# Performance work log

Measured on AMD Instinct MI355X. Metric: run time of the kernel, lower is better.

Reference implementation:

```python
import jax, jax.numpy as jnp
import numpy as np

BETA = 1.0  # temperature; label_softmax=True


def _criterion(pred, labels):
    # pred, labels: [M, W]; KLDivLoss(log_softmax(pred*beta), softmax(labels*beta)), mean over dim 1
    log_pt = jax.nn.log_softmax(pred * BETA, axis=1)
    log_lab = jax.nn.log_softmax(labels * BETA, axis=1)
    lab = jnp.exp(log_lab)
    kl = lab * (log_lab - log_pt)
    return kl.mean(axis=1)  # [M]


def _topk_rate(epoch):
    # cosine rampdown from epoch-210 over 30 epochs, clipped to [0.8, 1]
    cur = float(np.clip(epoch - 210, 0.0, 30.0))
    r = 0.5 * (np.cos(np.pi * cur / 30.0) + 1.0)
    return float(np.clip(r, 0.8, 1.0))


def setup_inputs() -> dict:
    key = jax.random.key(0)
    ks = jax.random.split(key, 6)
    N, K, W = 1024, 17, 512  # batch, joints, SimCC bins (256*2)
    return {
        "pred_x": jax.random.normal(ks[0], (N, K, W), jnp.float32),
        "pred_y": jax.random.normal(ks[1], (N, K, W), jnp.float32),
        "gt_x": jax.random.normal(ks[2], (N, K, W), jnp.float32),
        "gt_y": jax.random.normal(ks[3], (N, K, W), jnp.float32),
        "target_weight": jax.random.uniform(ks[4], (N, K), jnp.float32),
        "use_labels": jax.random.randint(ks[5], (N,), 0, 2),
        "epoch": 225,
    }


def reference(pred_x, pred_y, gt_x, gt_y, target_weight, use_labels, epoch):
    N, K, _ = pred_x.shape
    # target_weight_real: keep rows where use_labels == 0, else zero
    weight_real = (target_weight * (use_labels == 0).astype(target_weight.dtype)[:, None]).reshape(-1)
    rate = _topk_rate(int(epoch))
    num_visible = int(jnp.count_nonzero(target_weight))
    k = int(num_visible * rate)  # static k for top-k (data-dependent, computed eagerly)

    loss_all = jnp.zeros((), pred_x.dtype)
    weight_outs = []
    for pred, gt in ((pred_x, gt_x), (pred_y, gt_y)):
        p2 = pred.reshape(-1, pred.shape[-1])   # [N*K, W]
        t2 = gt.reshape(-1, gt.shape[-1])       # [N*K, W]
        # detached pass used only to pick the k smallest per-joint losses
        loss_small = _criterion(jax.lax.stop_gradient(p2), jax.lax.stop_gradient(t2))  # [N*K]
        loss_bat = loss_small.reshape(N, K)
        loss_new = jnp.where(target_weight > 0, loss_bat, loss_small.max())
        _, topk_idx = jax.lax.top_k(-loss_new.reshape(-1), k)  # smallest-k indices
        mask = jnp.zeros(N * K, dtype=pred.dtype).at[topk_idx].set(1.0)
        # live pass (gradients flow through pred and gt)
        loss_sm_re = _criterion(p2, t2)  # [N*K]
        weight_all = 2.0 * weight_real + mask
        weight_outs.append(weight_all)
        loss_all = loss_all + (loss_sm_re * weight_all).sum()
    return (loss_all / K, weight_outs[0], weight_outs[1])
```

## Files before the change

kernel.cpp:

```cpp
#include <hip/hip_runtime.h>
#include <math.h>

#define EQCAP 2048
#define PI_D 3.141592653589793

__device__ inline float wred_max(float v) {
    #pragma unroll
    for (int o = 32; o; o >>= 1) v = fmaxf(v, __shfl_xor(v, o));
    return v;
}
__device__ inline float wred_sum(float v) {
    #pragma unroll
    for (int o = 32; o; o >>= 1) v += __shfl_xor(v, o);
    return v;
}
__device__ inline unsigned fflip(float f) {
    unsigned b = __float_as_uint(f);
    return (b & 0x80000000u) ? ~b : (b | 0x80000000u);
}

__global__ void k_init(double* acc, int* count, unsigned* gmax_u, int* eqc) {
    if (threadIdx.x == 0) {
        *acc = 0.0; *count = 0;
        gmax_u[0] = 0u; gmax_u[1] = 0u;
        eqc[0] = 0; eqc[1] = 0;
    }
}

__global__ __launch_bounds__(256) void k_loss(
    const float* __restrict__ px, const float* __restrict__ py,
    const float* __restrict__ gx, const float* __restrict__ gy,
    float* __restrict__ lossbuf, int M)
{
    int wid  = (blockIdx.x * blockDim.x + threadIdx.x) >> 6;
    int lane = threadIdx.x & 63;
    if (wid >= 2 * M) return;
    int ax  = wid >= M;
    int row = ax ? wid - M : wid;
    const float* p = ax ? py : px;
    const float* g = ax ? gy : gx;
    const float4* p4 = reinterpret_cast<const float4*>(p + (size_t)row * 512);
    const float4* g4 = reinterpret_cast<const float4*>(g + (size_t)row * 512);
    float4 pa = p4[lane], pb = p4[lane + 64];
    float4 ga = g4[lane], gb = g4[lane + 64];
    float pv[8] = {pa.x, pa.y, pa.z, pa.w, pb.x, pb.y, pb.z, pb.w};
    float gv[8] = {ga.x, ga.y, ga.z, ga.w, gb.x, gb.y, gb.z, gb.w};

    float mp = -INFINITY, mg = -INFINITY;
    #pragma unroll
    for (int i = 0; i < 8; i++) { mp = fmaxf(mp, pv[i]); mg = fmaxf(mg, gv[i]); }
    mp = wred_max(mp); mg = wred_max(mg);

    float sp = 0.f, sg = 0.f;
    #pragma unroll
    for (int i = 0; i < 8; i++) { sp += __expf(pv[i] - mp); sg += __expf(gv[i] - mg); }
    sp = wred_sum(sp); sg = wred_sum(sg);
    float lp = __logf(sp), lg = __logf(sg);

    float acc = 0.f;
    #pragma unroll
    for (int i = 0; i < 8; i++) {
        float lsg = (gv[i] - mg) - lg;
        float lsp = (pv[i] - mp) - lp;
        acc += __expf(lsg) * (lsg - lsp);
    }
    acc = wred_sum(acc);
    if (lane == 0) lossbuf[wid] = acc * (1.0f / 512.0f);
}

__global__ __launch_bounds__(256) void k_stats2(
    const float* __restrict__ tw, const float* __restrict__ lossbuf,
    int* __restrict__ count, unsigned* __restrict__ gmax_u, int M)
{
    int tid = threadIdx.x, lane = tid & 63, wv = tid >> 6;
    int j = blockIdx.x * 256 + tid;
    int c = 0; unsigned ux = 0u, uy = 0u;
    if (j < M) {
        c  = (tw[j] != 0.0f);
        ux = fflip(lossbuf[j]);
        uy = fflip(lossbuf[M + j]);
    }
    #pragma unroll
    for (int o = 32; o; o >>= 1) {
        c += __shfl_xor(c, o);
        ux = max(ux, (unsigned)__shfl_xor((int)ux, o));
        uy = max(uy, (unsigned)__shfl_xor((int)uy, o));
    }
    __shared__ int sc[4]; __shared__ unsigned sx[4], sy[4];
    if (lane == 0) { sc[wv] = c; sx[wv] = ux; sy[wv] = uy; }
    __syncthreads();
    if (tid == 0) {
        int cs = sc[0] + sc[1] + sc[2] + sc[3];
        unsigned xs = max(max(sx[0], sx[1]), max(sx[2], sx[3]));
        unsigned ys = max(max(sy[0], sy[1]), max(sy[2], sy[3]));
        if (cs) atomicAdd(count, cs);
        atomicMax(&gmax_u[0], xs);
        atomicMax(&gmax_u[1], ys);
    }
}

__global__ __launch_bounds__(1024) void k_select(
    const float* __restrict__ tw, const float* __restrict__ lossbuf,
    const int* __restrict__ count, const unsigned* __restrict__ gmax_u,
    const int* __restrict__ ep,
    int* __restrict__ ki, unsigned* __restrict__ thr_u, int* __restrict__ cless, int M)
{
    extern __shared__ unsigned keys[];
    int ax = blockIdx.x;
    int tid = threadIdx.x, lane = tid & 63, wv = tid >> 6;
    __shared__ int hist[256];
    __shared__ unsigned s_pref;
    __shared__ int s_kr, s_cl;
    __shared__ int wsum[4];

    if (tid == 0) {
        int c = *count;
        double cur = fmin(fmax((double)(ep[0] - 210), 0.0), 30.0);
        double r = 0.5 * (cos(PI_D * cur / 30.0) + 1.0);
        r = fmin(fmax(r, 0.8), 1.0);
        int k = (int)((double)c * r);
        s_kr = k; s_pref = 0u; s_cl = 0;
        if (ax == 0) *ki = k;
    }

    unsigned gmu = gmax_u[ax];
    const float* lb = lossbuf + (size_t)ax * M;
    for (int j = tid; j < M; j += 1024) {
        float t = tw[j];
        float l = lb[j];
        keys[j] = (t > 0.f) ? fflip(l) : gmu;
    }
    __syncthreads();

    int k0 = s_kr;
    if (k0 <= 0) { if (tid == 0) { thr_u[ax] = 0u; cless[ax] = 0; } return; }

    const unsigned mhi[4] = {0x00000000u, 0xFF000000u, 0xFFFF0000u, 0xFFFFFF00u};

    for (int pass = 0; pass < 4; ++pass) {
        int shift = 24 - 8 * pass;
        if (tid < 256) hist[tid] = 0;
        __syncthreads();
        unsigned m = mhi[pass];
        unsigned pref = s_pref;
        for (int j = tid; j < M; j += 1024) {
            unsigned v = keys[j];
            if ((v & m) == (pref & m)) atomicAdd(&hist[(v >> shift) & 255], 1);
        }
        __syncthreads();
        int kr = s_kr;
        int h = (tid < 256) ? hist[tid] : 0;
        int inc = h;
        #pragma unroll
        for (int o = 1; o < 64; o <<= 1) {
            int n = __shfl_up(inc, o);
            if (lane >= o) inc += n;
        }
        if (lane == 63 && wv < 4) wsum[wv] = inc;
        __syncthreads();
        if (tid < 256) {
            int off = 0;
            #pragma unroll
            for (int w = 0; w < 4; w++) if (w < wv) off += wsum[w];
            int incl = inc + off, excl = incl - h;
            if (excl < kr && incl >= kr) {
                s_pref |= ((unsigned)tid) << shift;
                s_kr = kr - excl;
                s_cl += excl;
            }
        }
        __syncthreads();
    }
    if (tid == 0) { thr_u[ax] = s_pref; cless[ax] = s_cl; }
}

__global__ __launch_bounds__(256) void k_weight(
    const float* __restrict__ tw, const int* __restrict__ ul,
    const float* __restrict__ lossbuf, const unsigned* __restrict__ gmax_u,
    float* __restrict__ outw, const int* __restrict__ ki,
    const unsigned* __restrict__ thr_u, int* __restrict__ eqc,
    int* __restrict__ eqlist, double* __restrict__ acc, int M, int Kj)
{
    int ax = blockIdx.y;
    int m = blockIdx.x * blockDim.x + threadIdx.x;
    double contrib = 0.0;
    if (m < M) {
        int k = *ki;
        float mask = 0.f;
        unsigned v = (tw[m] > 0.f) ? fflip(lossbuf[(size_t)ax * M + m]) : gmax_u[ax];
        unsigned t = thr_u[ax];
        if (k > 0) {
            if (v < t) mask = 1.f;
            else if (v == t) {
                int pos = atomicAdd(&eqc[ax], 1);
                if (pos < EQCAP) eqlist[ax * EQCAP + pos] = m;
            }
        }
        float wr = (ul[m / Kj] == 0) ? tw[m] : 0.f;
        float wall = 2.f * wr + mask;
        outw[(size_t)ax * M + m] = wall;
        contrib = (double)lossbuf[(size_t)ax * M + m] * (double)wall;
    }
    #pragma unroll
    for (int o = 32; o; o >>= 1) contrib += __shfl_xor(contrib, o);
    __shared__ double s_c[4];
    int lane = threadIdx.x & 63, wv = threadIdx.x >> 6;
    if (lane == 0) s_c[wv] = contrib;
    __syncthreads();
    if (threadIdx.x == 0) atomicAdd(acc, s_c[0] + s_c[1] + s_c[2] + s_c[3]);
}

__global__ __launch_bounds__(256) void k_fix(
    float* __restrict__ outw, float* __restrict__ out0,
    const float* __restrict__ lossbuf, const int* __restrict__ ki,
    const int* __restrict__ cless, const int* __restrict__ eqc,
    const int* __restrict__ eqlist, const double* __restrict__ acc, int M, int Kj)
{
    __shared__ double s_c[4];
    int tid = threadIdx.x;
    double extra = 0.0;
    for (int ax = 0; ax < 2; ++ax) {
        int k = *ki;
        int ec = eqc[ax]; if (ec > EQCAP) ec = EQCAP;
        int need = (k > 0) ? (k - cless[ax]) : 0;
        if (need < 0) need = 0;
        if (need > ec) need = ec;
        if (need == ec) {
            for (int i = tid; i < ec; i += 256) {
                int m = eqlist[ax * EQCAP + i];
                outw[(size_t)ax * M + m] += 1.f;
                extra += (double)lossbuf[(size_t)ax * M + m];
            }
        } else if (tid == 0) {
            int last = -1;
            for (int s = 0; s < need; ++s) {
                int best = 0x7fffffff;
                for (int i = 0; i < ec; i++) {
                    int v = eqlist[ax * EQCAP + i];
                    if (v > last && v < best) best = v;
                }
                last = best;
                outw[(size_t)ax * M + best] += 1.f;
                extra += (double)lossbuf[(size_t)ax * M + best];
            }
        }
        __syncthreads();
    }
    #pragma unroll
    for (int o = 32; o; o >>= 1) extra += __shfl_xor(extra, o);
    int lane = tid & 63, wv = tid >> 6;
    if (lane == 0) s_c[wv] = extra;
    __syncthreads();
    if (tid == 0)
        out0[0] = (float)((acc[0] + s_c[0] + s_c[1] + s_c[2] + s_c[3]) / (double)Kj);
}

extern "C" void kernel_launch(void* const* d_in, const int* in_sizes, int n_in,
                              void* d_out, int out_size, void* d_ws, size_t ws_size,
                              hipStream_t stream)
{
    const float* px = (const float*)d_in[0];
    const float* py = (const float*)d_in[1];
    const float* gx = (const float*)d_in[2];
    const float* gy = (const float*)d_in[3];
    const float* tw = (const float*)d_in[4];
    const int*   ul = (const int*)d_in[5];
    const int*   ep = (const int*)d_in[6];

    int M  = in_sizes[4];
    int N  = in_sizes[5];
    int Kj = M / N;

    float* out  = (float*)d_out;
    float* out0 = out;
    float* outw = out + 1;

    char* ws = (char*)d_ws;
    double*   acc     = (double*)(ws + 0);
    int*      ki      = (int*)(ws + 8);
    int*      count   = (int*)(ws + 12);
    unsigned* gmax_u  = (unsigned*)(ws + 16);
    unsigned* thr_u   = (unsigned*)(ws + 24);
    int*      cless   = (int*)(ws + 32);
    int*      eqc     = (int*)(ws + 40);
    float*    lossbuf = (float*)(ws + 64);
    int*      eqlist  = (int*)(ws + 64 + (size_t)8 * M);

    k_init<<<1, 64, 0, stream>>>(acc, count, gmax_u, eqc);

    int nwaves = 2 * M;
    k_loss<<<(nwaves + 3) / 4, 256, 0, stream>>>(px, py, gx, gy, lossbuf, M);

    k_stats2<<<(M + 255) / 256, 256, 0, stream>>>(tw, lossbuf, count, gmax_u, M);

    size_t lds_bytes = (size_t)M * sizeof(unsigned);
    k_select<<<2, 1024, lds_bytes, stream>>>(tw, lossbuf, count, gmax_u, ep,
                                             ki, thr_u, cless, M);

    dim3 g4((M + 255) / 256, 2);
    k_weight<<<g4, 256, 0, stream>>>(tw, ul, lossbuf, gmax_u, outw, ki, thr_u,
                                     eqc, eqlist, acc, M, Kj);

    k_fix<<<1, 256, 0, stream>>>(outw, out0, lossbuf, ki, cless, eqc, eqlist, acc, M, Kj);
}
```

Baseline: 204.7 us.

## Fuse stats reduction into loss kernel and process x/y rows per wave

The per-row loss kernel now handles the x and y axes for the same row in one wave, with the max and sum reductions interleaved four or two at a time. It also absorbs the separate stats kernel by doing per-row atomicMax on the flipped loss bits and atomicAdd for the visible count directly from lane 0. This removes one kernel launch and a reread of lossbuf, and raises memory-level parallelism per wave. In exchange it issues many more global atomics, one per row rather than one per block, which could cause contention on two addresses.

```diff
diff --git a/kernel.cpp b/kernel.cpp
--- a/kernel.cpp
+++ b/kernel.cpp
@@ -4,15 +4,30 @@
 #define EQCAP 2048
 #define PI_D 3.141592653589793
 
-__device__ inline float wred_max(float v) {
-    #pragma unroll
-    for (int o = 32; o; o >>= 1) v = fmaxf(v, __shfl_xor(v, o));
-    return v;
-}
-__device__ inline float wred_sum(float v) {
-    #pragma unroll
-    for (int o = 32; o; o >>= 1) v += __shfl_xor(v, o);
-    return v;
+__device__ inline void wred_max4(float& a, float& b, float& c, float& d) {
+    #pragma unroll
+    for (int o = 32; o; o >>= 1) {
+        a = fmaxf(a, __shfl_xor(a, o));
+        b = fmaxf(b, __shfl_xor(b, o));
+        c = fmaxf(c, __shfl_xor(c, o));
+        d = fmaxf(d, __shfl_xor(d, o));
+    }
+}
+__device__ inline void wred_sum4(float& a, float& b, float& c, float& d) {
+    #pragma unroll
+    for (int o = 32; o; o >>= 1) {
+        a += __shfl_xor(a, o);
+        b += __shfl_xor(b, o);
+        c += __shfl_xor(c, o);
+        d += __shfl_xor(d, o);
+    }
+}
+__device__ inline void wred_sum2(float& a, float& b) {
+    #pragma unroll
+    for (int o = 32; o; o >>= 1) {
+        a += __shfl_xor(a, o);
+        b += __shfl_xor(b, o);
+    }
 }
 __device__ inline unsigned fflip(float f) {
     unsigned b = __float_as_uint(f);
@@ -27,75 +42,68 @@
     }
 }
 
-__global__ __launch_bounds__(256) void k_loss(
+__global__ __launch_bounds__(256, 4) void k_loss(
     const float* __restrict__ px, const float* __restrict__ py,
     const float* __restrict__ gx, const float* __restrict__ gy,
-    float* __restrict__ lossbuf, int M)
-{
-    int wid  = (blockIdx.x * blockDim.x + threadIdx.x) >> 6;
+    const float* __restrict__ tw, float* __restrict__ lossbuf,
+    int* __restrict__ count, unsigned* __restrict__ gmax_u, int M)
+{
+    int row  = (blockIdx.x * blockDim.x + threadIdx.x) >> 6;
     int lane = threadIdx.x & 63;
-    if (wid >= 2 * M) return;
-    int ax  = wid >= M;
-    int row = ax ? wid - M : wid;
-    const float* p = ax ? py : px;
-    const float* g = ax ? gy : gx;
-    const float4* p4 = reinterpret_cast<const float4*>(p + (size_t)row * 512);
-    const float4* g4 = reinterpret_cast<const float4*>(g + (size_t)row * 512);
-    float4 pa = p4[lane], pb = p4[lane + 64];
-    float4 ga = g4[lane], gb = g4[lane + 64];
-    float pv[8] = {pa.x, pa.y, pa.z, pa.w, pb.x, pb.y, pb.z, pb.w};
-    float gv[8] = {ga.x, ga.y, ga.z, ga.w, gb.x, gb.y, gb.z, gb.w};
-
-    float mp = -INFINITY, mg = -INFINITY;
-    #pragma unroll
-    for (int i = 0; i < 8; i++) { mp = fmaxf(mp, pv[i]); mg = fmaxf(mg, gv[i]); }
-    mp = wred_max(mp); mg = wred_max(mg);
-
-    float sp = 0.f, sg = 0.f;
-    #pragma unroll
-    for (int i = 0; i < 8; i++) { sp += __expf(pv[i] - mp); sg += __expf(gv[i] - mg); }
-    sp = wred_sum(sp); sg = wred_sum(sg);
-    float lp = __logf(sp), lg = __logf(sg);
-
-    float acc = 0.f;
+    if (row >= M) return;
+    size_t base = (size_t)row * 512;
+    const float4* x4 = reinterpret_cast<const float4*>(px + base);
+    const float4* y4 = reinterpret_cast<const float4*>(py + base);
+    const float4* u4 = reinterpret_cast<const float4*>(gx + base);
+    const float4* v4 = reinterpret_cast<const float4*>(gy + base);
+    float4 xA = x4[lane], xB = x4[lane + 64];
+    float4 uA = u4[lane], uB = u4[lane + 64];
+    float4 yA = y4[lane], yB = y4[lane + 64];
+    float4 vA = v4[lane], vB = v4[lane + 64];
+
+    float pX[8] = {xA.x, xA.y, xA.z, xA.w, xB.x, xB.y, xB.z, xB.w};
+    float gX[8] = {uA.x, uA.y, uA.z, uA.w, uB.x, uB.y, uB.z, uB.w};
+    float pY[8] = {yA.x, yA.y, yA.z, yA.w, yB.x, yB.y, yB.z, yB.w};
+    float gY[8] = {vA.x, vA.y, vA.z, vA.w, vB.x, vB.y, vB.z, vB.w};
+
+    float mpX = -INFINITY, mgX = -INFINITY, mpY = -INFINITY, mgY = -INFINITY;
     #pragma unroll
     for (int i = 0; i < 8; i++) {
-        float lsg = (gv[i] - mg) - lg;
-        float lsp = (pv[i] - mp) - lp;
-        acc += __expf(lsg) * (lsg - lsp);
-    }
-    acc = wred_sum(acc);
-    if (lane == 0) lossbuf[wid] = acc * (1.0f / 512.0f);
-}
-
-__global__ __launch_bounds__(256) void k_stats2(
-    const float* __restrict__ tw, const float* __restrict__ lossbuf,
-    int* __restrict__ count, unsigned* __restrict__ gmax_u, int M)
-{
-    int tid = threadIdx.x, lane = tid & 63, wv = tid >> 6;
-    int j = blockIdx.x * 256 + tid;
-    int c = 0; unsigned ux = 0u, uy = 0u;
-    if (j < M) {
-        c  = (tw[j] != 0.0f);
-        ux = fflip(lossbuf[j]);
-        uy = fflip(lossbuf[M + j]);
-    }
-    #pragma unroll
-    for (int o = 32; o; o >>= 1) {
-        c += __shfl_xor(c, o);
-        ux = max(ux, (unsigned)__shfl_xor((int)ux, o));
-        uy = max(uy, (unsigned)__shfl_xor((int)uy, o));
-    }
-    __shared__ int sc[4]; __shared__ unsigned sx[4], sy[4];
-    if (lane == 0) { sc[wv] = c; sx[wv] = ux; sy[wv] = uy; }
-    __syncthreads();
-    if (tid == 0) {
-        int cs = sc[0] + sc[1] + sc[2] + sc[3];
-        unsigned xs = max(max(sx[0], sx[1]), max(sx[2], sx[3]));
-        unsigned ys = max(max(sy[0], sy[1]), max(sy[2], sy[3]));
-        if (cs) atomicAdd(count, cs);
-        atomicMax(&gmax_u[0], xs);
-        atomicMax(&gmax_u[1], ys);
+        mpX = fmaxf(mpX, pX[i]); mgX = fmaxf(mgX, gX[i]);
+        mpY = fmaxf(mpY, pY[i]); mgY = fmaxf(mgY, gY[i]);
+    }
+    wred_max4(mpX, mgX, mpY, mgY);
+
+    float sPX = 0.f, sGX = 0.f, sPY = 0.f, sGY = 0.f;
+    #pragma unroll
+    for (int i = 0; i < 8; i++) {
+        sPX += __expf(pX[i] - mpX); sGX += __expf(gX[i] - mgX);
+        sPY += __expf(pY[i] - mpY); sGY += __expf(gY[i] - mgY);
+    }
+    wred_sum4(sPX, sGX, sPY, sGY);
+    float lPX = __logf(sPX), lGX = __logf(sGX);
+    float lPY = __logf(sPY), lGY = __logf(sGY);
+
+    float aX = 0.f, aY = 0.f;
+    #pragma unroll
+    for (int i = 0; i < 8; i++) {
+        float lsgX = (gX[i] - mgX) - lGX;
+        float lspX = (pX[i] - mpX) - lPX;
+        aX += __expf(lsgX) * (lsgX - lspX);
+        float lsgY = (gY[i] - mgY) - lGY;
+        float lspY = (pY[i] - mpY) - lPY;
+        aY += __expf(lsgY) * (lsgY - lspY);
+    }
+    wred_sum2(aX, aY);
+
+    if (lane == 0) {
+        float lx = aX * (1.0f / 512.0f);
+        float ly = aY * (1.0f / 512.0f);
+        lossbuf[row]     = lx;
+        lossbuf[M + row] = ly;
+        atomicMax(&gmax_u[0], fflip(lx));
+        atomicMax(&gmax_u[1], fflip(ly));
+        if (tw[row] != 0.0f) atomicAdd(count, 1);
     }
 }
 
@@ -288,10 +296,9 @@
 
     k_init<<<1, 64, 0, stream>>>(acc, count, gmax_u, eqc);
 
-    int nwaves = 2 * M;
-    k_loss<<<(nwaves + 3) / 4, 256, 0, stream>>>(px, py, gx, gy, lossbuf, M);
-
-    k_stats2<<<(M + 255) / 256, 256, 0, stream>>>(tw, lossbuf, count, gmax_u, M);
+    int blocks = (M * 64 + 255) / 256;
+    k_loss<<<blocks, 256, 0, stream>>>(px, py, gx, gy, tw, lossbuf,
+                                       count, gmax_u, M);
 
     size_t lds_bytes = (size_t)M * sizeof(unsigned);
     k_select<<<2, 1024, lds_bytes, stream>>>(tw, lossbuf, count, gmax_u, ep,
```

After: 758.6 us. 271% more time.
